# Kernel tuning notes

Measured on AMD Instinct MI355X. Metric: run time of the kernel, lower is better.

## Reference

```python
import jax, jax.numpy as jnp
import numpy as np

EMBED_DIM = 256
NUM_HEADS = 8
N_Q = 300    # num queries
HW = 4096    # flattened key/value tokens
B = 16       # batch


def _linear(x, W, b):
    # torch nn.Linear: y = x @ W^T + b ; W is [out, in]
    return jnp.einsum('lbc,dc->lbd', x, W) + b


def setup_inputs() -> dict:
    key = jax.random.key(0)
    ks = jax.random.split(key, 32)
    C = EMBED_DIM
    s = 1.0 / np.sqrt(C)
    inp = {
        'query': jax.random.normal(ks[0], (N_Q, B, C), jnp.float32),
        'key': jax.random.normal(ks[1], (HW, B, C), jnp.float32),
        'value': jax.random.normal(ks[2], (HW, B, C), jnp.float32),
        'query_pos': jax.random.normal(ks[3], (N_Q, B, C), jnp.float32),
        'key_pos': jax.random.normal(ks[4], (HW, B, C), jnp.float32),
        'query_sine_embed': jax.random.normal(ks[5], (N_Q, B, C), jnp.float32),
    }
    names = ['qc', 'qp', 'qs', 'kc', 'kp', 'v', 'o']
    for i, nm in enumerate(names):
        inp[f'W_{nm}'] = jax.random.uniform(ks[6 + 2 * i], (C, C), jnp.float32, -s, s)
        inp[f'b_{nm}'] = jax.random.uniform(ks[7 + 2 * i], (C,), jnp.float32, -s, s)
    return inp


def reference(query, key, value, query_pos, key_pos, query_sine_embed,
              W_qc, b_qc, W_qp, b_qp, W_qs, b_qs, W_kc, b_kc,
              W_kp, b_kp, W_v, b_v, W_o, b_o):
    H = NUM_HEADS
    N, Bc, C = query.shape
    L = key.shape[0]
    Dh = C // H
    identity = query

    query_content = _linear(query, W_qc, b_qc)          # [N,B,C]
    key_content = _linear(key, W_kc, b_kc)              # [L,B,C]
    v = _linear(value, W_v, b_v)                        # [L,B,C]
    kp = _linear(key_pos, W_kp, b_kp)                   # [L,B,C]
    # is_first_layer == True branch
    qp = _linear(query_pos, W_qp, b_qp)                 # [N,B,C]
    q = query_content + qp
    k = key_content + kp

    qs = _linear(query_sine_embed, W_qs, b_qs)          # [N,B,C]
    # concat content and positional halves per head -> head dim 2*Dh
    q = jnp.concatenate([q.reshape(N, Bc, H, Dh), qs.reshape(N, Bc, H, Dh)], axis=3)
    k = jnp.concatenate([k.reshape(L, Bc, H, Dh), kp.reshape(L, Bc, H, Dh)], axis=3)

    q = q.transpose(1, 2, 0, 3)                          # [B,H,N,2Dh]
    k = k.transpose(1, 2, 0, 3)                          # [B,H,L,2Dh]
    v = v.reshape(L, Bc, H, Dh).transpose(1, 2, 0, 3)    # [B,H,L,Dh]

    scale = (2 * Dh) ** (-0.5)
    attn = jnp.einsum('bhnd,bhld->bhnl', q * scale, k)   # [B,H,N,L]
    attn = jax.nn.softmax(attn, axis=-1)
    out = jnp.einsum('bhnl,bhld->bhnd', attn, v)         # [B,H,N,Dh]
    out = out.transpose(0, 2, 1, 3).reshape(Bc, N, C)    # [B,N,C]
    out = jnp.einsum('bnc,dc->bnd', out, W_o) + b_o
    out = out.transpose(1, 0, 2)                         # [N,B,C]
    return identity + out
```

## Files before the change

kernel.cpp:

```cpp
#include <hip/hip_runtime.h>
#include <cstdint>
#include <cstddef>


typedef float  f4  __attribute__((ext_vector_type(4)));
typedef __bf16 b8v __attribute__((ext_vector_type(8)));

#define MFMA_BF16(a, b, c) __builtin_amdgcn_mfma_f32_16x16x32_bf16((a), (b), (c), 0, 0, 0)

#define GLD_LDS16(gp, lp)                                             \
  __builtin_amdgcn_global_load_lds(                                   \
      (const __attribute__((address_space(1))) void*)(gp),            \
      (__attribute__((address_space(3))) void*)(lp), 16, 0, 0)

__global__ __launch_bounds__(256) void convert_w(
    const float* __restrict__ W0, const float* __restrict__ W1,
    const float* __restrict__ W2, __bf16* __restrict__ Wbf)
{
  int i = blockIdx.x * 256 + threadIdx.x;
  int base = i * 4;
  int m = base >> 16;
  int off = base & 65535;
  const float* W = (m == 0) ? W0 : (m == 1) ? W1 : W2;
  float4 v = *(const float4*)(W + off);
  __bf16 o[4];
  o[0] = (__bf16)v.x; o[1] = (__bf16)v.y; o[2] = (__bf16)v.z; o[3] = (__bf16)v.w;
  *(uint2*)(Wbf + (size_t)m * 65536 + off) = *(uint2*)o;
}

__global__ __launch_bounds__(256, 2) void key_side_gemm(
    const float* __restrict__ key, const float* __restrict__ key_pos,
    const float* __restrict__ value, const __bf16* __restrict__ Wbf,
    const float* __restrict__ b_kc, const float* __restrict__ b_kp,
    const float* __restrict__ b_v,
    __bf16* __restrict__ K64, __bf16* __restrict__ V32)
{
  __shared__ char smem[65536];
  const int tid  = threadIdx.x;
  const int wave = tid >> 6, lane = tid & 63;
  const int lrow = lane & 15, quad = lane >> 4;
  const int p  = blockIdx.y;
  const int r0 = blockIdx.x * 128;
  const int rowbase = (wave & 1) * 64;
  const int colbase = (wave >> 1) * 128;

  const float* __restrict__ X = (p == 0) ? key : (p == 1) ? key_pos : value;
  const __bf16* __restrict__ Wb = Wbf + (size_t)p * 65536;
  const float* __restrict__ bias = (p == 0) ? b_kc : (p == 1) ? b_kp : b_v;

  auto stageW = [&](int buf, int kc) {
#pragma unroll
    for (int it = 0; it < 8; ++it) {
      int slot = it * 256 + tid;
      int wr = slot >> 3, gp = slot & 7;
      int g  = gp ^ (wr & 7);
      GLD_LDS16(Wb + (size_t)wr * 256 + kc + g * 8, smem + buf * 32768 + slot * 16);
    }
  };
  auto readB = [&](int buf, int ct, int kk4) -> b8v {
    int wr = colbase + ct * 16 + lrow;
    int g  = (kk4 + quad) ^ (wr & 7);
    return *(const b8v*)(smem + buf * 32768 + wr * 128 + g * 16);
  };
  auto loadA = [&](float4* x0, float4* x1, int kc) {
#pragma unroll
    for (int rt = 0; rt < 4; ++rt) {
      const float* xp = X + (size_t)(r0 + rowbase + rt * 16 + lrow) * 256 + kc + quad * 8;
      x0[rt] = *(const float4*)xp;
      x1[rt] = *(const float4*)(xp + 4);
    }
  };
  auto mk = [&](float4 x0, float4 x1) -> b8v {
    b8v t;
    t[0] = (__bf16)x0.x; t[1] = (__bf16)x0.y; t[2] = (__bf16)x0.z; t[3] = (__bf16)x0.w;
    t[4] = (__bf16)x1.x; t[5] = (__bf16)x1.y; t[6] = (__bf16)x1.z; t[7] = (__bf16)x1.w;
    return t;
  };

  f4 acc[4][8];
#pragma unroll
  for (int i = 0; i < 4; ++i)
#pragma unroll
    for (int j = 0; j < 8; ++j) acc[i][j] = f4{0.f, 0.f, 0.f, 0.f};

  float4 c0[4], c1[4], d0[4], d1[4];
  loadA(c0, c1, 0);
  stageW(0, 0);
  __syncthreads();

  for (int s = 0; s < 4; ++s) {
    const int kc0 = s * 64, buf = s & 1;
    loadA(d0, d1, kc0 + 32);
    if (s < 3) stageW(buf ^ 1, kc0 + 64);

    b8v a[4];
#pragma unroll
    for (int rt = 0; rt < 4; ++rt) a[rt] = mk(c0[rt], c1[rt]);
#pragma unroll
    for (int ct = 0; ct < 8; ++ct) {
      b8v bfr = readB(buf, ct, 0);
#pragma unroll
      for (int rt = 0; rt < 4; ++rt) acc[rt][ct] = MFMA_BF16(a[rt], bfr, acc[rt][ct]);
    }

    if (s < 3) loadA(c0, c1, kc0 + 64);

#pragma unroll
    for (int rt = 0; rt < 4; ++rt) a[rt] = mk(d0[rt], d1[rt]);
#pragma unroll
    for (int ct = 0; ct < 8; ++ct) {
      b8v bfr = readB(buf, ct, 4);
#pragma unroll
      for (int rt = 0; rt < 4; ++rt) acc[rt][ct] = MFMA_BF16(a[rt], bfr, acc[rt][ct]);
    }
    __syncthreads();
  }

  __bf16* Os = (__bf16*)smem;
#pragma unroll
  for (int ct = 0; ct < 8; ++ct) {
    int col = colbase + ct * 16 + lrow;
    float bv = bias[col];
#pragma unroll
    for (int rt = 0; rt < 4; ++rt)
#pragma unroll
      for (int r = 0; r < 4; ++r) {
        int row = rowbase + rt * 16 + quad * 4 + r;
        Os[row * 256 + col] = (__bf16)(acc[rt][ct][r] + bv);
      }
  }
  __syncthreads();
#pragma unroll
  for (int it = 0; it < 16; ++it) {
    int chunk = it * 64 + wave * 16 + (lane & 15);
    int q = lane >> 4;
    int row = chunk >> 3, h = chunk & 7;
    int R = r0 + row, l = R >> 4, bb = R & 15;
    uint4 v = *(const uint4*)(Os + chunk * 32 + q * 8);
    __bf16* dst = (p == 2) ? (V32 + ((size_t)(bb * 8 + h) * 4096 + l) * 32)
                           : (K64 + ((size_t)(bb * 8 + h) * 4096 + l) * 64 + p * 32);
    *(uint4*)(dst + q * 8) = v;
  }
}

__global__ __launch_bounds__(256) void query_side_gemm(
    const float* __restrict__ query, const float* __restrict__ query_pos,
    const float* __restrict__ query_sine,
    const float* __restrict__ W_qc, const float* __restrict__ b_qc,
    const float* __restrict__ W_qp, const float* __restrict__ b_qp,
    const float* __restrict__ W_qs, const float* __restrict__ b_qs,
    __bf16* __restrict__ Q64)
{
  __shared__ __bf16 Ws[256][72];
  const int tid  = threadIdx.x;
  const int wave = tid >> 6, lane = tid & 63;
  const int lrow = lane & 15, quad = lane >> 4;
  const int r0 = blockIdx.x * 64;

  f4 acc[16];
#pragma unroll
  for (int i = 0; i < 16; ++i) acc[i] = f4{0.f, 0.f, 0.f, 0.f};

  for (int kc = 0; kc < 768; kc += 64) {
    const float* X; const float* W;
    if (kc < 256)      { X = query;      W = W_qc; }
    else if (kc < 512) { X = query_pos;  W = W_qp; }
    else               { X = query_sine; W = W_qs; }
    const int ko = kc & 255;
#pragma unroll
    for (int it = 0; it < 16; ++it) {
      int idx = it * 256 + tid;
      int row = idx >> 4, c4 = idx & 15;
      float4 w = *(const float4*)(W + (size_t)row * 256 + ko + c4 * 4);
      __bf16* dp = &Ws[row][c4 * 4];
      dp[0] = (__bf16)w.x; dp[1] = (__bf16)w.y; dp[2] = (__bf16)w.z; dp[3] = (__bf16)w.w;
    }
    __syncthreads();
#pragma unroll
    for (int kk = 0; kk < 64; kk += 32) {
      const float* xp = X + (size_t)(r0 + wave * 16 + lrow) * 256 + ko + kk + quad * 8;
      float4 x0 = *(const float4*)xp;
      float4 x1 = *(const float4*)(xp + 4);
      b8v a;
      a[0] = (__bf16)x0.x; a[1] = (__bf16)x0.y; a[2] = (__bf16)x0.z; a[3] = (__bf16)x0.w;
      a[4] = (__bf16)x1.x; a[5] = (__bf16)x1.y; a[6] = (__bf16)x1.z; a[7] = (__bf16)x1.w;
#pragma unroll
      for (int ct = 0; ct < 16; ++ct) {
        b8v bf = *(const b8v*)&Ws[ct * 16 + lrow][kk + quad * 8];
        acc[ct] = MFMA_BF16(a, bf, acc[ct]);
      }
    }
    __syncthreads();
    if (kc == 448) {
#pragma unroll
      for (int ct = 0; ct < 16; ++ct) {
        int col = ct * 16 + lrow;
        float bsum = b_qc[col] + b_qp[col];
        int h = col >> 5, d = col & 31;
#pragma unroll
        for (int r = 0; r < 4; ++r) {
          int row = r0 + wave * 16 + quad * 4 + r;
          int n = row >> 4, bb = row & 15;
          Q64[((size_t)(bb * 8 + h) * 320 + n) * 64 + d] = (__bf16)((acc[ct][r] + bsum) * 0.125f);
        }
      }
    }
  }
#pragma unroll
  for (int ct = 0; ct < 16; ++ct) {
    int col = ct * 16 + lrow;
    float bsum = b_qc[col] + b_qp[col] + b_qs[col];
    int h = col >> 5, d = col & 31;
#pragma unroll
    for (int r = 0; r < 4; ++r) {
      int row = r0 + wave * 16 + quad * 4 + r;
      int n = row >> 4, bb = row & 15;
      Q64[((size_t)(bb * 8 + h) * 320 + n) * 64 + 32 + d] = (__bf16)((acc[ct][r] + bsum) * 0.125f);
    }
  }
}

__global__ __launch_bounds__(256, 2) void attn_part(
    const __bf16* __restrict__ Q64, const __bf16* __restrict__ K64,
    const __bf16* __restrict__ V32,
    __bf16* __restrict__ Opart, float* __restrict__ Mpart, float* __restrict__ Lpart)
{
  __shared__ __bf16 Ks[128 * 64];
  __shared__ __bf16 Vt[32][136];
  __shared__ __bf16 Pt[4][16][136];
  const int tid  = threadIdx.x;
  const int wave = tid >> 6, lane = tid & 63;
  const int lrow = lane & 15, quad = lane >> 4;
  const int ls = blockIdx.x, bh = blockIdx.y;
  const int l0base = ls * 1024;

  const __bf16* Kb = K64 + (size_t)bh * 4096 * 64;
  const __bf16* Vb = V32 + (size_t)bh * 4096 * 32;

  b8v qa0[5], qa1[5];
#pragma unroll
  for (int t = 0; t < 5; ++t) {
    const __bf16* Qb = Q64 + ((size_t)bh * 320 + wave * 80 + t * 16 + lrow) * 64;
    qa0[t] = *(const b8v*)(Qb + quad * 8);
    qa1[t] = *(const b8v*)(Qb + 32 + quad * 8);
  }

  const int vs = tid & 3, vrh = tid >> 2;

  auto loadKV = [&](uint4* kr, uint4* vv, int c) {
    int l0 = l0base + c * 128;
#pragma unroll
    for (int it = 0; it < 4; ++it) {
      int slot = it * 256 + tid, row = slot >> 3, gs = slot & 7;
      int g = gs ^ (row & 7);
      kr[it] = *(const uint4*)(Kb + (size_t)(l0 + row) * 64 + g * 8);
    }
    vv[0] = *(const uint4*)(Vb + (size_t)(l0 + 2 * vrh) * 32 + vs * 8);
    vv[1] = *(const uint4*)(Vb + (size_t)(l0 + 2 * vrh + 1) * 32 + vs * 8);
  };
  auto stage = [&](const uint4* kr, const uint4* vv) {
#pragma unroll
    for (int it = 0; it < 4; ++it) {
      int slot = it * 256 + tid;
      *(uint4*)((char*)Ks + slot * 16) = kr[it];
    }
    __bf16 a[8], b[8];
    *(uint4*)a = vv[0]; *(uint4*)b = vv[1];
#pragma unroll
    for (int j = 0; j < 8; ++j) {
      __bf16 pr[2] = {a[j], b[j]};
      *(uint32_t*)&Vt[vs * 8 + j][2 * vrh] = *(const uint32_t*)pr;
    }
  };
  auto readKA = [&](int wr, int g) -> b8v {
    int gs = g ^ (wr & 7);
    return *(const b8v*)((const char*)Ks + wr * 128 + gs * 16);
  };

  float mst[5], lst[5];
  f4 oacc[5][2];
#pragma unroll
  for (int t = 0; t < 5; ++t) {
    mst[t] = -1e30f; lst[t] = 0.f;
    oacc[t][0] = f4{0.f, 0.f, 0.f, 0.f};
    oacc[t][1] = f4{0.f, 0.f, 0.f, 0.f};
  }

  auto compute = [&]() {
#pragma unroll
    for (int t = 0; t < 5; ++t) {
      f4 sc[8];
#pragma unroll
      for (int ct = 0; ct < 8; ++ct) {
        b8v ka0 = readKA(ct * 16 + lrow, quad);
        b8v ka1 = readKA(ct * 16 + lrow, 4 + quad);
        f4 z = f4{0.f, 0.f, 0.f, 0.f};
        z = MFMA_BF16(ka0, qa0[t], z);
        z = MFMA_BF16(ka1, qa1[t], z);
        sc[ct] = z;
      }
      float mx = sc[0][0];
#pragma unroll
      for (int ct = 0; ct < 8; ++ct)
#pragma unroll
        for (int r = 0; r < 4; ++r) mx = fmaxf(mx, sc[ct][r]);
      mx = fmaxf(mx, __shfl_xor(mx, 16));
      mx = fmaxf(mx, __shfl_xor(mx, 32));
      float mnew = fmaxf(mst[t], mx);
      float alpha = __expf(mst[t] - mnew);
      mst[t] = mnew;
      float rsum = 0.f;
#pragma unroll
      for (int ct = 0; ct < 8; ++ct)
#pragma unroll
        for (int r = 0; r < 4; ++r) {
          sc[ct][r] = __expf(sc[ct][r] - mnew);
          rsum += sc[ct][r];
        }
      rsum += __shfl_xor(rsum, 16);
      rsum += __shfl_xor(rsum, 32);
      lst[t] = lst[t] * alpha + rsum;
#pragma unroll
      for (int c2 = 0; c2 < 2; ++c2)
#pragma unroll
        for (int r = 0; r < 4; ++r) oacc[t][c2][r] *= alpha;

#pragma unroll
      for (int ct = 0; ct < 8; ++ct) {
        __bf16 p4[4];
#pragma unroll
        for (int r = 0; r < 4; ++r) p4[r] = (__bf16)sc[ct][r];
        *(uint2*)&Pt[wave][lrow][ct * 16 + quad * 4] = *(const uint2*)p4;
      }
#pragma unroll
      for (int kt = 0; kt < 4; ++kt) {
        b8v pb = *(const b8v*)&Pt[wave][lrow][kt * 32 + quad * 8];
#pragma unroll
        for (int c2 = 0; c2 < 2; ++c2) {
          b8v va = *(const b8v*)&Vt[c2 * 16 + lrow][kt * 32 + quad * 8];
          oacc[t][c2] = MFMA_BF16(va, pb, oacc[t][c2]);
        }
      }
    }
  };

  uint4 kA[4], vA[2], kB[4], vB[2];
  loadKV(kA, vA, 0);
  for (int c = 0; c < 8; c += 2) {
    __syncthreads();
    stage(kA, vA);
    loadKV(kB, vB, c + 1);
    __syncthreads();
    compute();
    __syncthreads();
    stage(kB, vB);
    if (c + 2 < 8) loadKV(kA, vA, c + 2);
    __syncthreads();
    compute();
  }

  const size_t pbase = ((size_t)bh * 4 + ls) * 320;
#pragma unroll
  for (int t = 0; t < 5; ++t) {
    int q = wave * 80 + t * 16 + lrow;
    float inv = 1.0f / lst[t];
#pragma unroll
    for (int c2 = 0; c2 < 2; ++c2) {
      __bf16 o4[4];
#pragma unroll
      for (int r = 0; r < 4; ++r) o4[r] = (__bf16)(oacc[t][c2][r] * inv);
      *(uint2*)&Opart[(pbase + q) * 32 + c2 * 16 + quad * 4] = *(const uint2*)o4;
    }
    if (quad == 0) {
      Mpart[pbase + q] = mst[t];
      Lpart[pbase + q] = lst[t];
    }
  }
}

__global__ __launch_bounds__(256) void attn_combine(
    const __bf16* __restrict__ Opart, const float* __restrict__ Mpart,
    const float* __restrict__ Lpart, __bf16* __restrict__ Obf)
{
  const int bh = blockIdx.y;
  const int idx = blockIdx.x * 256 + threadIdx.x;
  const int q = idx >> 5, d = idx & 31;
  if (q >= 300) return;
  const size_t rb = ((size_t)bh * 4) * 320 + q;
  float m0 = Mpart[rb], m1 = Mpart[rb + 320], m2 = Mpart[rb + 640], m3 = Mpart[rb + 960];
  float M = fmaxf(fmaxf(m0, m1), fmaxf(m2, m3));
  float w0 = Lpart[rb]       * __expf(m0 - M);
  float w1 = Lpart[rb + 320] * __expf(m1 - M);
  float w2 = Lpart[rb + 640] * __expf(m2 - M);
  float w3 = Lpart[rb + 960] * __expf(m3 - M);
  float S = w0 + w1 + w2 + w3;
  float o = w0 * (float)Opart[rb * 32 + d]
          + w1 * (float)Opart[(rb + 320) * 32 + d]
          + w2 * (float)Opart[(rb + 640) * 32 + d]
          + w3 * (float)Opart[(rb + 960) * 32 + d];
  int b = bh >> 3, h = bh & 7;
  Obf[((size_t)b * 300 + q) * 256 + h * 32 + d] = (__bf16)(o / S);
}

__global__ __launch_bounds__(256) void out_proj_gemm(
    const __bf16* __restrict__ Obf, const float* __restrict__ W_o,
    const float* __restrict__ b_o, const float* __restrict__ query,
    float* __restrict__ out)
{
  __shared__ __bf16 Ws[256][72];
  const int tid  = threadIdx.x;
  const int wave = tid >> 6, lane = tid & 63;
  const int lrow = lane & 15, quad = lane >> 4;
  const int r0 = blockIdx.x * 64;

  f4 acc[16];
#pragma unroll
  for (int i = 0; i < 16; ++i) acc[i] = f4{0.f, 0.f, 0.f, 0.f};

  for (int kc0 = 0; kc0 < 256; kc0 += 64) {
#pragma unroll
    for (int it = 0; it < 16; ++it) {
      int idx = it * 256 + tid;
      int row = idx >> 4, c4 = idx & 15;
      float4 w = *(const float4*)(W_o + (size_t)row * 256 + kc0 + c4 * 4);
      __bf16* dp = &Ws[row][c4 * 4];
      dp[0] = (__bf16)w.x; dp[1] = (__bf16)w.y; dp[2] = (__bf16)w.z; dp[3] = (__bf16)w.w;
    }
    __syncthreads();
#pragma unroll
    for (int kk = 0; kk < 64; kk += 32) {
      b8v a = *(const b8v*)(Obf + (size_t)(r0 + wave * 16 + lrow) * 256 + kc0 + kk + quad * 8);
#pragma unroll
      for (int ct = 0; ct < 16; ++ct) {
        b8v bf = *(const b8v*)&Ws[ct * 16 + lrow][kk + quad * 8];
        acc[ct] = MFMA_BF16(a, bf, acc[ct]);
      }
    }
    __syncthreads();
  }
#pragma unroll
  for (int ct = 0; ct < 16; ++ct) {
    int col = ct * 16 + lrow;
    float bo = b_o[col];
#pragma unroll
    for (int r = 0; r < 4; ++r) {
      int row = r0 + wave * 16 + quad * 4 + r;
      int bb = row / 300, n = row % 300;
      size_t oaddr = ((size_t)n * 16 + bb) * 256 + col;
      out[oaddr] = acc[ct][r] + bo + query[oaddr];
    }
  }
}

extern "C" void kernel_launch(void* const* d_in, const int* in_sizes, int n_in,
                              void* d_out, int out_size, void* d_ws, size_t ws_size,
                              hipStream_t stream) {
  (void)in_sizes; (void)n_in; (void)out_size; (void)ws_size;
  const float* query      = (const float*)d_in[0];
  const float* key        = (const float*)d_in[1];
  const float* value      = (const float*)d_in[2];
  const float* query_pos  = (const float*)d_in[3];
  const float* key_pos    = (const float*)d_in[4];
  const float* query_sine = (const float*)d_in[5];
  const float* W_qc = (const float*)d_in[6];  const float* b_qc = (const float*)d_in[7];
  const float* W_qp = (const float*)d_in[8];  const float* b_qp = (const float*)d_in[9];
  const float* W_qs = (const float*)d_in[10]; const float* b_qs = (const float*)d_in[11];
  const float* W_kc = (const float*)d_in[12]; const float* b_kc = (const float*)d_in[13];
  const float* W_kp = (const float*)d_in[14]; const float* b_kp = (const float*)d_in[15];
  const float* W_v  = (const float*)d_in[16]; const float* b_v  = (const float*)d_in[17];
  const float* W_o  = (const float*)d_in[18]; const float* b_o  = (const float*)d_in[19];
  float* out = (float*)d_out;

  char* ws = (char*)d_ws;
  constexpr size_t K64_BYTES = (size_t)128 * 4096 * 64 * 2;
  constexpr size_t V32_BYTES = (size_t)128 * 4096 * 32 * 2;
  constexpr size_t Q64_BYTES = (size_t)128 * 320 * 64 * 2;
  constexpr size_t OBF_BYTES = (size_t)16 * 300 * 256 * 2;
  constexpr size_t WBF_BYTES = (size_t)3 * 256 * 256 * 2;
  constexpr size_t OPART_BYTES = (size_t)128 * 4 * 320 * 32 * 2;
  constexpr size_t MPART_BYTES = (size_t)128 * 4 * 320 * 4;
  __bf16* K64 = (__bf16*)ws;
  __bf16* V32 = (__bf16*)(ws + K64_BYTES);
  __bf16* Q64 = (__bf16*)(ws + K64_BYTES + V32_BYTES);
  __bf16* Obf = (__bf16*)(ws + K64_BYTES + V32_BYTES + Q64_BYTES);
  __bf16* Wbf = (__bf16*)(ws + K64_BYTES + V32_BYTES + Q64_BYTES + OBF_BYTES);
  char*  pbase = ws + K64_BYTES + V32_BYTES + Q64_BYTES + OBF_BYTES + WBF_BYTES;
  __bf16* Opart = (__bf16*)pbase;
  float*  Mpart = (float*)(pbase + OPART_BYTES);
  float*  Lpart = (float*)(pbase + OPART_BYTES + MPART_BYTES);

  hipLaunchKernelGGL(convert_w, dim3(192), dim3(256), 0, stream,
                     W_kc, W_kp, W_v, Wbf);
  hipLaunchKernelGGL(key_side_gemm, dim3(512, 3), dim3(256), 0, stream,
                     key, key_pos, value, Wbf, b_kc, b_kp, b_v, K64, V32);
  hipLaunchKernelGGL(query_side_gemm, dim3(75), dim3(256), 0, stream,
                     query, query_pos, query_sine, W_qc, b_qc, W_qp, b_qp, W_qs, b_qs, Q64);
  hipLaunchKernelGGL(attn_part, dim3(4, 128), dim3(256), 0, stream,
                     Q64, K64, V32, Opart, Mpart, Lpart);
  hipLaunchKernelGGL(attn_combine, dim3(40, 128), dim3(256), 0, stream,
                     Opart, Mpart, Lpart, Obf);
  hipLaunchKernelGGL(out_proj_gemm, dim3(75), dim3(256), 0, stream,
                     Obf, W_o, b_o, query, out);
}
```

Measured before the change: 461.0 us.

## Split K into separate content/pos planes and tile key GEMM per batch for contiguous stores

The key-side GEMM now assigns each block 128 consecutive tokens of a single batch rather than 128 consecutive flattened rows that interleave batches. Its output stores therefore write contiguous 64-byte runs per head into separate planes for the content and positional halves of K, using an XOR-swizzled LDS staging buffer to avoid bank conflicts. The attention kernel then gathers each K row from the two planes. The aim is to coalesce the scattered bf16 stores of the K/V projection, at the cost of strided input row reads (stride 16*256 floats) and a branchy two-plane address in the attention K loads.

```diff
diff --git a/kernel.cpp b/kernel.cpp
--- a/kernel.cpp
+++ b/kernel.cpp
@@ -12,6 +12,8 @@
   __builtin_amdgcn_global_load_lds(                                   \
       (const __attribute__((address_space(1))) void*)(gp),            \
       (__attribute__((address_space(3))) void*)(lp), 16, 0, 0)
+
+#define KPLANE ((size_t)128 * 4096 * 32)
 
 __global__ __launch_bounds__(256) void convert_w(
     const float* __restrict__ W0, const float* __restrict__ W1,
@@ -40,7 +42,9 @@
   const int wave = tid >> 6, lane = tid & 63;
   const int lrow = lane & 15, quad = lane >> 4;
   const int p  = blockIdx.y;
-  const int r0 = blockIdx.x * 128;
+  const int lc = blockIdx.x >> 4;
+  const int batch = blockIdx.x & 15;
+  const int l0 = lc * 128;
   const int rowbase = (wave & 1) * 64;
   const int colbase = (wave >> 1) * 128;
 
@@ -65,7 +69,8 @@
   auto loadA = [&](float4* x0, float4* x1, int kc) {
 #pragma unroll
     for (int rt = 0; rt < 4; ++rt) {
-      const float* xp = X + (size_t)(r0 + rowbase + rt * 16 + lrow) * 256 + kc + quad * 8;
+      const float* xp = X + ((size_t)(l0 + rowbase + rt * 16 + lrow) * 16 + batch) * 256
+                          + kc + quad * 8;
       x0[rt] = *(const float4*)xp;
       x1[rt] = *(const float4*)(xp + 4);
     }
@@ -121,25 +126,27 @@
   for (int ct = 0; ct < 8; ++ct) {
     int col = colbase + ct * 16 + lrow;
     float bv = bias[col];
+    int cg = col >> 3, cr = col & 7;
 #pragma unroll
     for (int rt = 0; rt < 4; ++rt)
 #pragma unroll
       for (int r = 0; r < 4; ++r) {
         int row = rowbase + rt * 16 + quad * 4 + r;
-        Os[row * 256 + col] = (__bf16)(acc[rt][ct][r] + bv);
+        int g = cg ^ ((row ^ (row >> 3)) & 7);
+        Os[row * 256 + g * 8 + cr] = (__bf16)(acc[rt][ct][r] + bv);
       }
   }
   __syncthreads();
 #pragma unroll
   for (int it = 0; it < 16; ++it) {
-    int chunk = it * 64 + wave * 16 + (lane & 15);
-    int q = lane >> 4;
-    int row = chunk >> 3, h = chunk & 7;
-    int R = r0 + row, l = R >> 4, bb = R & 15;
-    uint4 v = *(const uint4*)(Os + chunk * 32 + q * 8);
-    __bf16* dst = (p == 2) ? (V32 + ((size_t)(bb * 8 + h) * 4096 + l) * 32)
-                           : (K64 + ((size_t)(bb * 8 + h) * 4096 + l) * 64 + p * 32);
-    *(uint4*)(dst + q * 8) = v;
+    int h   = it >> 1;
+    int row = (it & 1) * 64 + (tid >> 2);
+    int seg = tid & 3;
+    int g = (h * 4 + seg) ^ ((row ^ (row >> 3)) & 7);
+    uint4 v = *(const uint4*)(Os + row * 256 + g * 8);
+    size_t rowidx = ((size_t)(batch * 8 + h) * 4096) + l0 + row;
+    if (p == 2) *(uint4*)(V32 + rowidx * 32 + seg * 8) = v;
+    else        *(uint4*)(K64 + (size_t)p * KPLANE + rowidx * 32 + seg * 8) = v;
   }
 }
 
@@ -234,8 +241,9 @@
   const int ls = blockIdx.x, bh = blockIdx.y;
   const int l0base = ls * 1024;
 
-  const __bf16* Kb = K64 + (size_t)bh * 4096 * 64;
-  const __bf16* Vb = V32 + (size_t)bh * 4096 * 32;
+  const __bf16* Kb0 = K64 + (size_t)bh * 4096 * 32;
+  const __bf16* Kb1 = Kb0 + KPLANE;
+  const __bf16* Vb  = V32 + (size_t)bh * 4096 * 32;
 
   b8v qa0[5], qa1[5];
 #pragma unroll
@@ -253,7 +261,10 @@
     for (int it = 0; it < 4; ++it) {
       int slot = it * 256 + tid, row = slot >> 3, gs = slot & 7;
       int g = gs ^ (row & 7);
-      kr[it] = *(const uint4*)(Kb + (size_t)(l0 + row) * 64 + g * 8);
+      const __bf16* src = (g < 4)
+          ? (Kb0 + (size_t)(l0 + row) * 32 + g * 8)
+          : (Kb1 + (size_t)(l0 + row) * 32 + (g - 4) * 8);
+      kr[it] = *(const uint4*)src;
     }
     vv[0] = *(const uint4*)(Vb + (size_t)(l0 + 2 * vrh) * 32 + vs * 8);
     vv[1] = *(const uint4*)(Vb + (size_t)(l0 + 2 * vrh + 1) * 32 + vs * 8);
```

New measurement: 460.9 us. Within noise of the previous version (-0.0%).

## Fuse key/value projections into attention kernel per head slice

Applied to the files above, without the earlier changes.

Removes the separate key-side GEMM and its bf16 K/V workspace. The attention kernel now projects each 128-row chunk of key, key_pos and value on the fly, using the per-head slice of the weights staged through LDS. This avoids writing and re-reading the projected K/V tensors. In exchange, every head's block re-reads the fp32 inputs for its batch, and the projection runs with small tiles and extra barriers inside the attention loop.

```diff
diff --git a/kernel.cpp b/kernel.cpp
--- a/kernel.cpp
+++ b/kernel.cpp
@@ -14,133 +14,21 @@
       (__attribute__((address_space(3))) void*)(lp), 16, 0, 0)
 
 __global__ __launch_bounds__(256) void convert_w(
-    const float* __restrict__ W0, const float* __restrict__ W1,
-    const float* __restrict__ W2, __bf16* __restrict__ Wbf)
+    const float* __restrict__ W_kc, const float* __restrict__ W_kp,
+    const float* __restrict__ W_v, __bf16* __restrict__ Wslice)
 {
   int i = blockIdx.x * 256 + threadIdx.x;
   int base = i * 4;
-  int m = base >> 16;
-  int off = base & 65535;
-  const float* W = (m == 0) ? W0 : (m == 1) ? W1 : W2;
-  float4 v = *(const float4*)(W + off);
+  int h = base / 24576;
+  int rem = base - h * 24576;
+  int j = rem >> 8;
+  int k = rem & 255;
+  const float* W = (j < 32) ? W_kc : (j < 64) ? W_kp : W_v;
+  int r = j & 31;
+  float4 v = *(const float4*)(W + (size_t)(h * 32 + r) * 256 + k);
   __bf16 o[4];
   o[0] = (__bf16)v.x; o[1] = (__bf16)v.y; o[2] = (__bf16)v.z; o[3] = (__bf16)v.w;
-  *(uint2*)(Wbf + (size_t)m * 65536 + off) = *(uint2*)o;
-}
-
-__global__ __launch_bounds__(256, 2) void key_side_gemm(
-    const float* __restrict__ key, const float* __restrict__ key_pos,
-    const float* __restrict__ value, const __bf16* __restrict__ Wbf,
-    const float* __restrict__ b_kc, const float* __restrict__ b_kp,
-    const float* __restrict__ b_v,
-    __bf16* __restrict__ K64, __bf16* __restrict__ V32)
-{
-  __shared__ char smem[65536];
-  const int tid  = threadIdx.x;
-  const int wave = tid >> 6, lane = tid & 63;
-  const int lrow = lane & 15, quad = lane >> 4;
-  const int p  = blockIdx.y;
-  const int r0 = blockIdx.x * 128;
-  const int rowbase = (wave & 1) * 64;
-  const int colbase = (wave >> 1) * 128;
-
-  const float* __restrict__ X = (p == 0) ? key : (p == 1) ? key_pos : value;
-  const __bf16* __restrict__ Wb = Wbf + (size_t)p * 65536;
-  const float* __restrict__ bias = (p == 0) ? b_kc : (p == 1) ? b_kp : b_v;
-
-  auto stageW = [&](int buf, int kc) {
-#pragma unroll
-    for (int it = 0; it < 8; ++it) {
-      int slot = it * 256 + tid;
-      int wr = slot >> 3, gp = slot & 7;
-      int g  = gp ^ (wr & 7);
-      GLD_LDS16(Wb + (size_t)wr * 256 + kc + g * 8, smem + buf * 32768 + slot * 16);
-    }
-  };
-  auto readB = [&](int buf, int ct, int kk4) -> b8v {
-    int wr = colbase + ct * 16 + lrow;
-    int g  = (kk4 + quad) ^ (wr & 7);
-    return *(const b8v*)(smem + buf * 32768 + wr * 128 + g * 16);
-  };
-  auto loadA = [&](float4* x0, float4* x1, int kc) {
-#pragma unroll
-    for (int rt = 0; rt < 4; ++rt) {
-      const float* xp = X + (size_t)(r0 + rowbase + rt * 16 + lrow) * 256 + kc + quad * 8;
-      x0[rt] = *(const float4*)xp;
-      x1[rt] = *(const float4*)(xp + 4);
-    }
-  };
-  auto mk = [&](float4 x0, float4 x1) -> b8v {
-    b8v t;
-    t[0] = (__bf16)x0.x; t[1] = (__bf16)x0.y; t[2] = (__bf16)x0.z; t[3] = (__bf16)x0.w;
-    t[4] = (__bf16)x1.x; t[5] = (__bf16)x1.y; t[6] = (__bf16)x1.z; t[7] = (__bf16)x1.w;
-    return t;
-  };
-
-  f4 acc[4][8];
-#pragma unroll
-  for (int i = 0; i < 4; ++i)
-#pragma unroll
-    for (int j = 0; j < 8; ++j) acc[i][j] = f4{0.f, 0.f, 0.f, 0.f};
-
-  float4 c0[4], c1[4], d0[4], d1[4];
-  loadA(c0, c1, 0);
-  stageW(0, 0);
-  __syncthreads();
-
-  for (int s = 0; s < 4; ++s) {
-    const int kc0 = s * 64, buf = s & 1;
-    loadA(d0, d1, kc0 + 32);
-    if (s < 3) stageW(buf ^ 1, kc0 + 64);
-
-    b8v a[4];
-#pragma unroll
-    for (int rt = 0; rt < 4; ++rt) a[rt] = mk(c0[rt], c1[rt]);
-#pragma unroll
-    for (int ct = 0; ct < 8; ++ct) {
-      b8v bfr = readB(buf, ct, 0);
-#pragma unroll
-      for (int rt = 0; rt < 4; ++rt) acc[rt][ct] = MFMA_BF16(a[rt], bfr, acc[rt][ct]);
-    }
-
-    if (s < 3) loadA(c0, c1, kc0 + 64);
-
-#pragma unroll
-    for (int rt = 0; rt < 4; ++rt) a[rt] = mk(d0[rt], d1[rt]);
-#pragma unroll
-    for (int ct = 0; ct < 8; ++ct) {
-      b8v bfr = readB(buf, ct, 4);
-#pragma unroll
-      for (int rt = 0; rt < 4; ++rt) acc[rt][ct] = MFMA_BF16(a[rt], bfr, acc[rt][ct]);
-    }
-    __syncthreads();
-  }
-
-  __bf16* Os = (__bf16*)smem;
-#pragma unroll
-  for (int ct = 0; ct < 8; ++ct) {
-    int col = colbase + ct * 16 + lrow;
-    float bv = bias[col];
-#pragma unroll
-    for (int rt = 0; rt < 4; ++rt)
-#pragma unroll
-      for (int r = 0; r < 4; ++r) {
-        int row = rowbase + rt * 16 + quad * 4 + r;
-        Os[row * 256 + col] = (__bf16)(acc[rt][ct][r] + bv);
-      }
-  }
-  __syncthreads();
-#pragma unroll
-  for (int it = 0; it < 16; ++it) {
-    int chunk = it * 64 + wave * 16 + (lane & 15);
-    int q = lane >> 4;
-    int row = chunk >> 3, h = chunk & 7;
-    int R = r0 + row, l = R >> 4, bb = R & 15;
-    uint4 v = *(const uint4*)(Os + chunk * 32 + q * 8);
-    __bf16* dst = (p == 2) ? (V32 + ((size_t)(bb * 8 + h) * 4096 + l) * 32)
-                           : (K64 + ((size_t)(bb * 8 + h) * 4096 + l) * 64 + p * 32);
-    *(uint4*)(dst + q * 8) = v;
-  }
+  *(uint2*)(Wslice + base) = *(uint2*)o;
 }
 
 __global__ __launch_bounds__(256) void query_side_gemm(
@@ -220,11 +108,15 @@
   }
 }
 
-__global__ __launch_bounds__(256, 2) void attn_part(
-    const __bf16* __restrict__ Q64, const __bf16* __restrict__ K64,
-    const __bf16* __restrict__ V32,
+__global__ __launch_bounds__(256, 2) void proj_attn(
+    const float* __restrict__ key, const float* __restrict__ key_pos,
+    const float* __restrict__ value, const __bf16* __restrict__ Wslice,
+    const float* __restrict__ b_kc, const float* __restrict__ b_kp,
+    const float* __restrict__ b_v,
+    const __bf16* __restrict__ Q64,
     __bf16* __restrict__ Opart, float* __restrict__ Mpart, float* __restrict__ Lpart)
 {
+  __shared__ __bf16 Wsh[2][96 * 64];
   __shared__ __bf16 Ks[128 * 64];
   __shared__ __bf16 Vt[32][136];
   __shared__ __bf16 Pt[4][16][136];
@@ -232,10 +124,10 @@
   const int wave = tid >> 6, lane = tid & 63;
   const int lrow = lane & 15, quad = lane >> 4;
   const int ls = blockIdx.x, bh = blockIdx.y;
+  const int batch = bh >> 3, h = bh & 7;
   const int l0base = ls * 1024;
 
-  const __bf16* Kb = K64 + (size_t)bh * 4096 * 64;
-  const __bf16* Vb = V32 + (size_t)bh * 4096 * 32;
+  const __bf16* __restrict__ Wb = Wslice + (size_t)h * 96 * 256;
 
   b8v qa0[5], qa1[5];
 #pragma unroll
@@ -245,33 +137,88 @@
     qa1[t] = *(const b8v*)(Qb + 32 + quad * 8);
   }
 
-  const int vs = tid & 3, vrh = tid >> 2;
-
-  auto loadKV = [&](uint4* kr, uint4* vv, int c) {
-    int l0 = l0base + c * 128;
-#pragma unroll
-    for (int it = 0; it < 4; ++it) {
-      int slot = it * 256 + tid, row = slot >> 3, gs = slot & 7;
-      int g = gs ^ (row & 7);
-      kr[it] = *(const uint4*)(Kb + (size_t)(l0 + row) * 64 + g * 8);
-    }
-    vv[0] = *(const uint4*)(Vb + (size_t)(l0 + 2 * vrh) * 32 + vs * 8);
-    vv[1] = *(const uint4*)(Vb + (size_t)(l0 + 2 * vrh + 1) * 32 + vs * 8);
-  };
-  auto stage = [&](const uint4* kr, const uint4* vv) {
-#pragma unroll
-    for (int it = 0; it < 4; ++it) {
+  auto stageW = [&](int qt, int buf) {
+#pragma unroll
+    for (int it = 0; it < 3; ++it) {
       int slot = it * 256 + tid;
-      *(uint4*)((char*)Ks + slot * 16) = kr[it];
-    }
-    __bf16 a[8], b[8];
-    *(uint4*)a = vv[0]; *(uint4*)b = vv[1];
-#pragma unroll
-    for (int j = 0; j < 8; ++j) {
-      __bf16 pr[2] = {a[j], b[j]};
-      *(uint32_t*)&Vt[vs * 8 + j][2 * vrh] = *(const uint32_t*)pr;
-    }
-  };
+      int j = slot >> 3, gp = slot & 7;
+      int g = gp ^ (j & 7);
+      GLD_LDS16(Wb + (size_t)j * 256 + qt * 64 + g * 8,
+                (char*)&Wsh[buf][0] + slot * 16);
+    }
+  };
+  auto readW = [&](int buf, int n, int G) -> b8v {
+    int gs = G ^ (n & 7);
+    return *(const b8v*)((const char*)&Wsh[buf][0] + n * 128 + gs * 16);
+  };
+  auto mk = [&](float4 x0, float4 x1) -> b8v {
+    b8v t;
+    t[0] = (__bf16)x0.x; t[1] = (__bf16)x0.y; t[2] = (__bf16)x0.z; t[3] = (__bf16)x0.w;
+    t[4] = (__bf16)x1.x; t[5] = (__bf16)x1.y; t[6] = (__bf16)x1.z; t[7] = (__bf16)x1.w;
+    return t;
+  };
+
+  f4 pacc[3][2][2];
+#pragma unroll
+  for (int m = 0; m < 3; ++m)
+#pragma unroll
+    for (int i = 0; i < 2; ++i)
+#pragma unroll
+      for (int j = 0; j < 2; ++j) pacc[m][i][j] = f4{0.f, 0.f, 0.f, 0.f};
+
+  auto projq = [&](int c, int qt, int buf) {
+#pragma unroll
+    for (int m = 0; m < 3; ++m) {
+      const float* __restrict__ X = (m == 0) ? key : (m == 1) ? key_pos : value;
+#pragma unroll
+      for (int ks = 0; ks < 2; ++ks) {
+#pragma unroll
+        for (int rt = 0; rt < 2; ++rt) {
+          int row = l0base + c * 128 + wave * 32 + rt * 16 + lrow;
+          const float* xp = X + ((size_t)row * 16 + batch) * 256
+                              + qt * 64 + ks * 32 + quad * 8;
+          float4 x0 = *(const float4*)xp;
+          float4 x1 = *(const float4*)(xp + 4);
+          b8v a = mk(x0, x1);
+#pragma unroll
+          for (int ct = 0; ct < 2; ++ct) {
+            b8v bfr = readW(buf, m * 32 + ct * 16 + lrow, ks * 4 + quad);
+            pacc[m][rt][ct] = MFMA_BF16(a, bfr, pacc[m][rt][ct]);
+          }
+        }
+      }
+    }
+  };
+
+  auto writeKsVt = [&]() {
+#pragma unroll
+    for (int m = 0; m < 3; ++m) {
+      const float* __restrict__ bias = (m == 0) ? b_kc : (m == 1) ? b_kp : b_v;
+#pragma unroll
+      for (int ct = 0; ct < 2; ++ct) {
+        int col = ct * 16 + lrow;
+        float bv = bias[h * 32 + col];
+#pragma unroll
+        for (int rt = 0; rt < 2; ++rt) {
+#pragma unroll
+          for (int r = 0; r < 4; ++r) {
+            int l = wave * 32 + rt * 16 + quad * 4 + r;
+            float val = pacc[m][rt][ct][r] + bv;
+            if (m < 2) {
+              int glin = m * 4 + ct * 2 + (lrow >> 3);
+              *((__bf16*)((char*)Ks + l * 128 + ((glin ^ (l & 7)) * 16) + (col & 7) * 2))
+                  = (__bf16)val;
+            } else {
+              Vt[col][l] = (__bf16)val;
+            }
+          }
+        }
+#pragma unroll
+        for (int rt = 0; rt < 2; ++rt) pacc[m][rt][ct] = f4{0.f, 0.f, 0.f, 0.f};
+      }
+    }
+  };
+
   auto readKA = [&](int wr, int g) -> b8v {
     int gs = g ^ (wr & 7);
     return *(const b8v*)((const char*)Ks + wr * 128 + gs * 16);
@@ -344,19 +291,20 @@
     }
   };
 
-  uint4 kA[4], vA[2], kB[4], vB[2];
-  loadKV(kA, vA, 0);
-  for (int c = 0; c < 8; c += 2) {
-    __syncthreads();
-    stage(kA, vA);
-    loadKV(kB, vB, c + 1);
+  stageW(0, 0);
+  __syncthreads();
+  for (int c = 0; c < 8; ++c) {
+#pragma unroll
+    for (int qt = 0; qt < 4; ++qt) {
+      int buf = qt & 1;
+      stageW((qt + 1) & 3, buf ^ 1);
+      projq(c, qt, buf);
+      __syncthreads();
+    }
+    writeKsVt();
     __syncthreads();
     compute();
     __syncthreads();
-    stage(kB, vB);
-    if (c + 2 < 8) loadKV(kA, vA, c + 2);
-    __syncthreads();
-    compute();
   }
 
   const size_t pbase = ((size_t)bh * 4 + ls) * 320;
@@ -472,31 +420,26 @@
   float* out = (float*)d_out;
 
   char* ws = (char*)d_ws;
-  constexpr size_t K64_BYTES = (size_t)128 * 4096 * 64 * 2;
-  constexpr size_t V32_BYTES = (size_t)128 * 4096 * 32 * 2;
+  constexpr size_t WSL_BYTES = (size_t)8 * 96 * 256 * 2;
   constexpr size_t Q64_BYTES = (size_t)128 * 320 * 64 * 2;
   constexpr size_t OBF_BYTES = (size_t)16 * 300 * 256 * 2;
-  constexpr size_t WBF_BYTES = (size_t)3 * 256 * 256 * 2;
   constexpr size_t OPART_BYTES = (size_t)128 * 4 * 320 * 32 * 2;
   constexpr size_t MPART_BYTES = (size_t)128 * 4 * 320 * 4;
-  __bf16* K64 = (__bf16*)ws;
-  __bf16* V32 = (__bf16*)(ws + K64_BYTES);
-  __bf16* Q64 = (__bf16*)(ws + K64_BYTES + V32_BYTES);
-  __bf16* Obf = (__bf16*)(ws + K64_BYTES + V32_BYTES + Q64_BYTES);
-  __bf16* Wbf = (__bf16*)(ws + K64_BYTES + V32_BYTES + Q64_BYTES + OBF_BYTES);
-  char*  pbase = ws + K64_BYTES + V32_BYTES + Q64_BYTES + OBF_BYTES + WBF_BYTES;
+  __bf16* Wslice = (__bf16*)ws;
+  __bf16* Q64 = (__bf16*)(ws + WSL_BYTES);
+  __bf16* Obf = (__bf16*)(ws + WSL_BYTES + Q64_BYTES);
+  char*  pbase = ws + WSL_BYTES + Q64_BYTES + OBF_BYTES;
   __bf16* Opart = (__bf16*)pbase;
   float*  Mpart = (float*)(pbase + OPART_BYTES);
   float*  Lpart = (float*)(pbase + OPART_BYTES + MPART_BYTES);
 
   hipLaunchKernelGGL(convert_w, dim3(192), dim3(256), 0, stream,
-                     W_kc, W_kp, W_v, Wbf);
-  hipLaunchKernelGGL(key_side_gemm, dim3(512, 3), dim3(256), 0, stream,
-                     key, key_pos, value, Wbf, b_kc, b_kp, b_v, K64, V32);
+                     W_kc, W_kp, W_v, Wslice);
   hipLaunchKernelGGL(query_side_gemm, dim3(75), dim3(256), 0, stream,
                      query, query_pos, query_sine, W_qc, b_qc, W_qp, b_qp, W_qs, b_qs, Q64);
-  hipLaunchKernelGGL(attn_part, dim3(4, 128), dim3(256), 0, stream,
-                     Q64, K64, V32, Opart, Mpart, Lpart);
+  hipLaunchKernelGGL(proj_attn, dim3(4, 128), dim3(256), 0, stream,
+                     key, key_pos, value, Wslice, b_kc, b_kp, b_v, Q64,
+                     Opart, Mpart, Lpart);
   hipLaunchKernelGGL(attn_combine, dim3(40, 128), dim3(256), 0, stream,
                      Opart, Mpart, Lpart, Obf);
   hipLaunchKernelGGL(out_proj_gemm, dim3(75), dim3(256), 0, stream,
```

Result: slower. 655.2 us (+42.1%).
